# Kernel tuning notes

Hardware: AMD Instinct MI355X
Metric: run time of the kernel (lower is better)

Reference implementation:

```python
import jax, jax.numpy as jnp
import numpy as np

NUM_EXPERTS = 8


def setup_inputs() -> dict:
    key = jax.random.key(0)
    k1, k2 = jax.random.split(key)
    G, T, D, E = 4, 2048, 1024, NUM_EXPERTS
    token_inputs = jax.random.normal(k1, (G, T, D), dtype=jnp.float32)
    router_weight = jax.random.normal(k2, (E, D), dtype=jnp.float32) * 0.02
    router_bias = jnp.zeros((E,), dtype=jnp.float32)
    return {
        "token_inputs": token_inputs,
        "router_weight": router_weight,
        "router_bias": router_bias,
        "expert_capacity": 320,
    }


def _routing(probs, expert_capacities):
    """Experts-preferred assignment: experts pick tokens in order, each up to
    its capacity, from tokens not yet taken by earlier experts."""
    G, T, E = probs.shape
    max_cap = max(expert_capacities)
    dispatch = jnp.zeros((G, T, E, max_cap), dtype=jnp.int32)
    combine = jnp.zeros((G, T, E, max_cap), dtype=probs.dtype)
    available = jnp.ones((G, T), dtype=probs.dtype)  # 1 if token unassigned
    g_idx = jnp.arange(G)[:, None]
    for e, cap in enumerate(expert_capacities):  # static small loop over experts
        masked = probs[:, :, e] * available                 # [G, T]
        gate, idx = jax.lax.top_k(masked, cap)              # [G, cap]
        c_idx = jnp.arange(cap)[None, :]
        dispatch = dispatch.at[g_idx, idx, e, c_idx].set(1)
        combine = combine.at[g_idx, idx, e, c_idx].set(gate)
        available = available.at[g_idx, idx].set(0.0)       # chosen tokens now taken
    return dispatch, combine


def reference(token_inputs, router_weight, router_bias, expert_capacity):
    x = token_inputs.astype(jnp.float32)
    # router logits: [G, T, E]
    logits = jnp.einsum("gtd,ed->gte", x, router_weight) + router_bias
    probs = jax.nn.softmax(logits, axis=-1)
    capacities = [int(expert_capacity)] * NUM_EXPERTS
    dispatch_mask, combine_array = _routing(probs, capacities)
    # router z-loss: mean over groups*tokens of logsumexp(logits)^2
    log_z = jax.nn.logsumexp(logits, axis=-1)
    z_loss = jnp.sum(log_z ** 2) / (logits.shape[0] * logits.shape[1])
    auxiliary_loss = jnp.float32(0.0)
    router_causal_loss = jnp.float32(0.0)
    return dispatch_mask, combine_array, auxiliary_loss, z_loss, router_causal_loss
```

## Files before the change

kernel.cpp:

```cpp
#include <hip/hip_runtime.h>

#define NEXP 8
typedef unsigned long long u64;
typedef unsigned int u32;

__global__ __launch_bounds__(512) void probs_fill_kernel(
    const float* __restrict__ x,
    const float* __restrict__ w,
    const float* __restrict__ bias,
    float* __restrict__ probsT,
    double* __restrict__ zpart,
    int* __restrict__ flags,
    float* __restrict__ out,
    long long nout4,
    long long GT, int npb, int nfb)
{
    if (blockIdx.x == 0 && threadIdx.x < 8) flags[threadIdx.x] = 0;

    if ((int)blockIdx.x >= npb) {
        const int fb = (int)blockIdx.x - npb;
        const long long stride = (long long)nfb * 512;
        const float4 z = make_float4(0.f, 0.f, 0.f, 0.f);
        for (long long k = (long long)fb * 512 + threadIdx.x; k < nout4; k += stride) {
            reinterpret_cast<float4*>(out)[k] = z;
        }
        return;
    }

    __shared__ float wl[NEXP * 1024];
    __shared__ double zred[8];
    for (int i = threadIdx.x; i < NEXP * 1024 / 4; i += 512) {
        reinterpret_cast<float4*>(wl)[i] = reinterpret_cast<const float4*>(w)[i];
    }
    __syncthreads();

    const int wave = threadIdx.x >> 6;
    const int lane = threadIdx.x & 63;
    const long long t = (long long)blockIdx.x * 8 + wave;
    const float* xr = x + t * 1024;

    float acc[NEXP];
#pragma unroll
    for (int e = 0; e < NEXP; ++e) acc[e] = 0.f;

#pragma unroll
    for (int c = 0; c < 4; ++c) {
        const int d = c * 256 + lane * 4;
        const float4 xv = *reinterpret_cast<const float4*>(xr + d);
#pragma unroll
        for (int e = 0; e < NEXP; ++e) {
            const float4 wv = *reinterpret_cast<const float4*>(wl + e * 1024 + d);
            acc[e] = fmaf(xv.x, wv.x, acc[e]);
            acc[e] = fmaf(xv.y, wv.y, acc[e]);
            acc[e] = fmaf(xv.z, wv.z, acc[e]);
            acc[e] = fmaf(xv.w, wv.w, acc[e]);
        }
    }
#pragma unroll
    for (int e = 0; e < NEXP; ++e) {
#pragma unroll
        for (int off = 32; off; off >>= 1) acc[e] += __shfl_xor(acc[e], off, 64);
    }

    if (lane == 0) {
        double l[NEXP];
        double mx = -1e300;
#pragma unroll
        for (int e = 0; e < NEXP; ++e) {
            l[e] = (double)acc[e] + (double)bias[e];
            mx = fmax(mx, l[e]);
        }
        double ex[NEXP];
        double s = 0.0;
#pragma unroll
        for (int e = 0; e < NEXP; ++e) { ex[e] = exp(l[e] - mx); s += ex[e]; }
        const double inv = 1.0 / s;
#pragma unroll
        for (int e = 0; e < NEXP; ++e) probsT[(long long)e * GT + t] = (float)(ex[e] * inv);
        const double lse = mx + log(s);
        zred[wave] = lse * lse;
    }
    __syncthreads();
    if (threadIdx.x == 0) {
        double s = 0.0;
#pragma unroll
        for (int i = 0; i < 8; ++i) s += zred[i];
        zpart[blockIdx.x] = s;
    }
}

#define NRANK 256

union __align__(16) Smem2 {
    struct { u64 keys[2048]; int part[1024]; } b;
    struct { int avail[2048]; int cnt[32]; int cnt2[32]; } c;
};

__global__ __launch_bounds__(1024) void rank_assign_kernel(
    const float* __restrict__ probsT,
    u64* __restrict__ skey,
    int* __restrict__ flags,
    const double* __restrict__ zpart,
    int nzpart,
    float* __restrict__ out,
    int T, int G, int cap, long long GT)
{
    __shared__ Smem2 sm;
    const int b = blockIdx.x;
    const int tid = threadIdx.x;
    const int lane = tid & 63;
    const int wv = tid >> 6;

    if (b < NRANK) {
        const int pair = b >> 3;
        const int sub  = b & 7;
        const int e = pair / G;
        const int g = pair - e * G;
        const float* p = probsT + (long long)e * GT + (long long)g * T;
        for (int j = tid; j < 2048; j += 1024)
            sm.b.keys[j] = ((u64)__float_as_uint(p[j]) << 32) | (u32)(~(u32)j);
        __syncthreads();
        const int slot = tid & 255;
        const int q = tid >> 8;
        const u64 kt = sm.b.keys[sub * 256 + slot];
        const ulonglong2* k2 = reinterpret_cast<const ulonglong2*>(sm.b.keys) + q * 256;
        int r = 0;
#pragma unroll 8
        for (int j = 0; j < 256; ++j) {
            const ulonglong2 v = k2[j];
            r += (v.x > kt); r += (v.y > kt);
        }
        sm.b.part[tid] = r;
        __syncthreads();
        if (tid < 256) {
            const int rank = sm.b.part[tid] + sm.b.part[tid + 256] + sm.b.part[tid + 512] + sm.b.part[tid + 768];
            skey[(long long)pair * T + rank] = sm.b.keys[sub * 256 + tid];
        }
        __syncthreads();
        if (tid == 0) { __threadfence(); atomicAdd(&flags[g], 1); }
        return;
    }

    const int g = b - NRANK;
    if (tid == 0) {
        while (__hip_atomic_load(&flags[g], __ATOMIC_RELAXED, __HIP_MEMORY_SCOPE_AGENT) < 64)
            __builtin_amdgcn_s_sleep(2);
        __threadfence();
    }
    __syncthreads();

    u64 ka[NEXP], kb[NEXP];
#pragma unroll
    for (int e = 0; e < NEXP; ++e) {
        const long long base = (long long)(e * G + g) * T;
        ka[e] = skey[base + tid];
        kb[e] = skey[base + tid + 1024];
    }
    sm.c.avail[tid] = 1;
    sm.c.avail[tid + 1024] = 1;

    float* dispatch = out;
    float* combine  = out + GT * (long long)NEXP * cap;
    const long long gbase = (long long)g * T;
    const u64 lmask = (lane == 0) ? 0ull : ((~0ull) >> (64 - lane));

    for (int e = 0; e < NEXP; ++e) {
        __syncthreads();
        const u64 k0 = ka[e], k1 = kb[e];
        const u32 idx0 = ~(u32)k0, idx1 = ~(u32)k1;
        const float v0 = __uint_as_float((u32)(k0 >> 32));
        const float v1 = __uint_as_float((u32)(k1 >> 32));
        const int f0 = sm.c.avail[idx0];
        const int f1 = sm.c.avail[idx1];
        const u64 m0 = __ballot(f0);
        const u64 m1 = __ballot(f1);
        if (lane == 0) { sm.c.cnt[wv] = __popcll(m0); sm.c.cnt[16 + wv] = __popcll(m1); }
        __syncthreads();
        int vi = (lane < 32) ? sm.c.cnt[lane] : 0;
#pragma unroll
        for (int o = 1; o < 32; o <<= 1) { const int t2 = __shfl_up(vi, o, 64); if (lane >= o) vi += t2; }
        const int off0 = wv ? __shfl(vi, wv - 1, 64) : 0;
        const int off1 = __shfl(vi, 15 + wv, 64);
        const int S    = __shfl(vi, 31, 64);
        const int pre0 = off0 + __popcll(m0 & lmask);
        const int pre1 = off1 + __popcll(m1 & lmask);
        const bool s0 = f0 && (pre0 < cap);
        const bool s1 = f1 && (pre1 < cap);
        if (s0) { const long long o_ = ((gbase + idx0) * NEXP + e) * (long long)cap + pre0; dispatch[o_] = 1.0f; combine[o_] = v0; }
        if (s1) { const long long o_ = ((gbase + idx1) * NEXP + e) * (long long)cap + pre1; dispatch[o_] = 1.0f; combine[o_] = v1; }
        if (S < cap) {
            const int u0 = 1 - sm.c.avail[tid];
            const int u1 = 1 - sm.c.avail[tid + 1024];
            const u64 n0 = __ballot(u0);
            const u64 n1 = __ballot(u1);
            if (lane == 0) { sm.c.cnt2[wv] = __popcll(n0); sm.c.cnt2[16 + wv] = __popcll(n1); }
            __syncthreads();
            int vj = (lane < 32) ? sm.c.cnt2[lane] : 0;
#pragma unroll
            for (int o = 1; o < 32; o <<= 1) { const int t2 = __shfl_up(vj, o, 64); if (lane >= o) vj += t2; }
            const int qoff0 = wv ? __shfl(vj, wv - 1, 64) : 0;
            const int qoff1 = __shfl(vj, 15 + wv, 64);
            const int q0 = qoff0 + __popcll(n0 & lmask);
            const int q1 = qoff1 + __popcll(n1 & lmask);
            const int nfill = cap - S;
            if (u0 && q0 < nfill) { const long long o_ = ((gbase + tid) * NEXP + e) * (long long)cap + S + q0; dispatch[o_] = 1.0f; }
            if (u1 && q1 < nfill) { const long long o_ = ((gbase + tid + 1024) * NEXP + e) * (long long)cap + S + q1; dispatch[o_] = 1.0f; }
        }
        if (s0) sm.c.avail[idx0] = 0;
        if (s1) sm.c.avail[idx1] = 0;
    }

    if (g == 0 && tid < 64) {
        double s = 0.0;
        for (int i = tid; i < nzpart; i += 64) s += zpart[i];
#pragma unroll
        for (int o = 32; o; o >>= 1) s += __shfl_xor(s, o, 64);
        if (tid == 0) {
            float* sc = out + 2 * GT * (long long)NEXP * cap;
            sc[0] = 0.0f;
            sc[1] = (float)(s / (double)GT);
            sc[2] = 0.0f;
        }
    }
}

extern "C" void kernel_launch(void* const* d_in, const int* in_sizes, int n_in,
                              void* d_out, int out_size, void* d_ws, size_t ws_size,
                              hipStream_t stream) {
    (void)n_in; (void)ws_size;
    const float* x    = (const float*)d_in[0];
    const float* w    = (const float*)d_in[1];
    const float* bias = (const float*)d_in[2];

    const int E = in_sizes[2];
    const int D = in_sizes[1] / E;
    const long long GT = (long long)in_sizes[0] / D;
    const int T = 2048;
    const int G = (int)(GT / T);
    const int cap = (int)(((long long)out_size - 3) / (2 * GT * E));
    const int npb = (int)(GT / 8);
    const int nfb = 2048;

    int*    flags  = (int*)d_ws;
    double* zpart  = (double*)((char*)d_ws + 4096);
    float*  probsT = (float*)((char*)d_ws + 16384);
    u64*    skey   = (u64*)((char*)d_ws + 16384 + (size_t)E * GT * sizeof(float));

    const long long nout4 = ((long long)out_size - 3) >> 2;

    probs_fill_kernel<<<npb + nfb, 512, 0, stream>>>(
        x, w, bias, probsT, zpart, flags, (float*)d_out, nout4, GT, npb, nfb);

    rank_assign_kernel<<<NRANK + G, 1024, 0, stream>>>(
        probsT, skey, flags, zpart, npb, (float*)d_out, T, G, cap, GT);
}
```

Baseline: 71.15 us.

## Split output zero-fill across kernels and buffer assignments in LDS

The output zero-fill is split. The first kernel clears only the first 3/8 of the output, and 256 extra blocks in the second kernel clear the rest while the ranking and assignment work runs. The assign blocks no longer write dispatch and combine inside the expert loop. They record each (value, index) entry in an LDS buffer, wait on a flag counter until all fill blocks finish, then scatter the entries. This overlaps the memset traffic with the serial routing work, at the cost of extra LDS use, a cross-block spin-wait, and the split ratio chosen by hand.

```diff
diff --git a/kernel.cpp b/kernel.cpp
--- a/kernel.cpp
+++ b/kernel.cpp
@@ -1,6 +1,9 @@
 #include <hip/hip_runtime.h>
 
 #define NEXP 8
+#define NRANK 256
+#define NFB2 256
+#define MAXCAP 512
 typedef unsigned long long u64;
 typedef unsigned int u32;
 
@@ -12,7 +15,7 @@
     double* __restrict__ zpart,
     int* __restrict__ flags,
     float* __restrict__ out,
-    long long nout4,
+    long long split4,
     long long GT, int npb, int nfb)
 {
     if (blockIdx.x == 0 && threadIdx.x < 8) flags[threadIdx.x] = 0;
@@ -21,7 +24,7 @@
         const int fb = (int)blockIdx.x - npb;
         const long long stride = (long long)nfb * 512;
         const float4 z = make_float4(0.f, 0.f, 0.f, 0.f);
-        for (long long k = (long long)fb * 512 + threadIdx.x; k < nout4; k += stride) {
+        for (long long k = (long long)fb * 512 + threadIdx.x; k < split4; k += stride) {
             reinterpret_cast<float4*>(out)[k] = z;
         }
         return;
@@ -89,20 +92,20 @@
     }
 }
 
-#define NRANK 256
-
 union __align__(16) Smem2 {
     struct { u64 keys[2048]; int part[1024]; } b;
-    struct { int avail[2048]; int cnt[32]; int cnt2[32]; } c;
+    struct { int avail[2048]; int cnt[32]; int cnt2[32];
+             u64 cbuf[NEXP * MAXCAP]; } c;
 };
 
-__global__ __launch_bounds__(1024) void rank_assign_kernel(
+__global__ __launch_bounds__(1024) void rank_assign_fill_kernel(
     const float* __restrict__ probsT,
     u64* __restrict__ skey,
     int* __restrict__ flags,
     const double* __restrict__ zpart,
     int nzpart,
     float* __restrict__ out,
+    long long split4, long long nout4,
     int T, int G, int cap, long long GT)
 {
     __shared__ Smem2 sm;
@@ -110,6 +113,18 @@
     const int tid = threadIdx.x;
     const int lane = tid & 63;
     const int wv = tid >> 6;
+
+    if (b >= NRANK + G) {
+        const int fb = b - (NRANK + G);
+        const long long stride = (long long)NFB2 * 1024;
+        const float4 z = make_float4(0.f, 0.f, 0.f, 0.f);
+        for (long long k = split4 + (long long)fb * 1024 + tid; k < nout4; k += stride) {
+            reinterpret_cast<float4*>(out)[k] = z;
+        }
+        __syncthreads();
+        if (tid == 0) { __threadfence(); atomicAdd(&flags[4], 1); }
+        return;
+    }
 
     if (b < NRANK) {
         const int pair = b >> 3;
@@ -159,17 +174,12 @@
     sm.c.avail[tid] = 1;
     sm.c.avail[tid + 1024] = 1;
 
-    float* dispatch = out;
-    float* combine  = out + GT * (long long)NEXP * cap;
-    const long long gbase = (long long)g * T;
     const u64 lmask = (lane == 0) ? 0ull : ((~0ull) >> (64 - lane));
 
     for (int e = 0; e < NEXP; ++e) {
         __syncthreads();
         const u64 k0 = ka[e], k1 = kb[e];
         const u32 idx0 = ~(u32)k0, idx1 = ~(u32)k1;
-        const float v0 = __uint_as_float((u32)(k0 >> 32));
-        const float v1 = __uint_as_float((u32)(k1 >> 32));
         const int f0 = sm.c.avail[idx0];
         const int f1 = sm.c.avail[idx1];
         const u64 m0 = __ballot(f0);
@@ -186,8 +196,8 @@
         const int pre1 = off1 + __popcll(m1 & lmask);
         const bool s0 = f0 && (pre0 < cap);
         const bool s1 = f1 && (pre1 < cap);
-        if (s0) { const long long o_ = ((gbase + idx0) * NEXP + e) * (long long)cap + pre0; dispatch[o_] = 1.0f; combine[o_] = v0; }
-        if (s1) { const long long o_ = ((gbase + idx1) * NEXP + e) * (long long)cap + pre1; dispatch[o_] = 1.0f; combine[o_] = v1; }
+        if (s0) sm.c.cbuf[e * cap + pre0] = ((k0 >> 32) << 32) | (u64)idx0;
+        if (s1) sm.c.cbuf[e * cap + pre1] = ((k1 >> 32) << 32) | (u64)idx1;
         if (S < cap) {
             const int u0 = 1 - sm.c.avail[tid];
             const int u1 = 1 - sm.c.avail[tid + 1024];
@@ -203,12 +213,13 @@
             const int q0 = qoff0 + __popcll(n0 & lmask);
             const int q1 = qoff1 + __popcll(n1 & lmask);
             const int nfill = cap - S;
-            if (u0 && q0 < nfill) { const long long o_ = ((gbase + tid) * NEXP + e) * (long long)cap + S + q0; dispatch[o_] = 1.0f; }
-            if (u1 && q1 < nfill) { const long long o_ = ((gbase + tid + 1024) * NEXP + e) * (long long)cap + S + q1; dispatch[o_] = 1.0f; }
+            if (u0 && q0 < nfill) sm.c.cbuf[e * cap + S + q0] = (u64)(u32)tid;
+            if (u1 && q1 < nfill) sm.c.cbuf[e * cap + S + q1] = (u64)(u32)(tid + 1024);
         }
         if (s0) sm.c.avail[idx0] = 0;
         if (s1) sm.c.avail[idx1] = 0;
     }
+    __syncthreads();
 
     if (g == 0 && tid < 64) {
         double s = 0.0;
@@ -220,6 +231,28 @@
             sc[0] = 0.0f;
             sc[1] = (float)(s / (double)GT);
             sc[2] = 0.0f;
+        }
+    }
+
+    if (tid == 0) {
+        while (__hip_atomic_load(&flags[4], __ATOMIC_RELAXED, __HIP_MEMORY_SCOPE_AGENT) < NFB2)
+            __builtin_amdgcn_s_sleep(2);
+        __threadfence();
+    }
+    __syncthreads();
+
+    float* dispatch = out;
+    float* combine  = out + GT * (long long)NEXP * cap;
+    const long long gbase = (long long)g * T;
+#pragma unroll
+    for (int e = 0; e < NEXP; ++e) {
+        for (int c = tid; c < cap; c += 1024) {
+            const u64 en = sm.c.cbuf[e * cap + c];
+            const u32 idx = (u32)en;
+            const float val = __uint_as_float((u32)(en >> 32));
+            const long long o_ = ((gbase + idx) * NEXP + e) * (long long)cap + c;
+            dispatch[o_] = 1.0f;
+            combine[o_]  = val;
         }
     }
 }
@@ -247,10 +280,11 @@
     u64*    skey   = (u64*)((char*)d_ws + 16384 + (size_t)E * GT * sizeof(float));
 
     const long long nout4 = ((long long)out_size - 3) >> 2;
+    const long long split4 = (nout4 * 3) / 8;
 
     probs_fill_kernel<<<npb + nfb, 512, 0, stream>>>(
-        x, w, bias, probsT, zpart, flags, (float*)d_out, nout4, GT, npb, nfb);
-
-    rank_assign_kernel<<<NRANK + G, 1024, 0, stream>>>(
-        probsT, skey, flags, zpart, npb, (float*)d_out, T, G, cap, GT);
+        x, w, bias, probsT, zpart, flags, (float*)d_out, split4, GT, npb, nfb);
+
+    rank_assign_fill_kernel<<<NRANK + G + NFB2, 1024, 0, stream>>>(
+        probsT, skey, flags, zpart, npb, (float*)d_out, split4, nout4, T, G, cap, GT);
 }
```

Result: slower. 73.43 us (+3.2%).

## Run per-group greedy assignment on a single wavefront without block barriers

Applied to the files above, without the earlier changes.

The per-group assignment phase now runs on one 64-lane wave per group. Each expert's sorted keys are loaded into registers and processed in 32 chunks with running ballot prefix counts, replacing the 1024-thread version that needed several __syncthreads and cross-wave scans per expert. This removes barrier and shared-memory scan overhead from the serial expert loop, but each group's work is now serialized on a single wave and most of the block's threads return early. The z-loss block also zeroes any tail output elements not covered by the float4 fill.

```diff
diff --git a/kernel.cpp b/kernel.cpp
--- a/kernel.cpp
+++ b/kernel.cpp
@@ -1,6 +1,7 @@
 #include <hip/hip_runtime.h>
 
 #define NEXP 8
+#define NRANK 256
 typedef unsigned long long u64;
 typedef unsigned int u32;
 
@@ -89,11 +90,9 @@
     }
 }
 
-#define NRANK 256
-
 union __align__(16) Smem2 {
     struct { u64 keys[2048]; int part[1024]; } b;
-    struct { int avail[2048]; int cnt[32]; int cnt2[32]; } c;
+    struct { int avail[2048]; } c;
 };
 
 __global__ __launch_bounds__(1024) void rank_assign_kernel(
@@ -103,13 +102,12 @@
     const double* __restrict__ zpart,
     int nzpart,
     float* __restrict__ out,
+    long long nout4, int out_size,
     int T, int G, int cap, long long GT)
 {
     __shared__ Smem2 sm;
     const int b = blockIdx.x;
     const int tid = threadIdx.x;
-    const int lane = tid & 63;
-    const int wv = tid >> 6;
 
     if (b < NRANK) {
         const int pair = b >> 3;
@@ -123,11 +121,11 @@
         const int slot = tid & 255;
         const int q = tid >> 8;
         const u64 kt = sm.b.keys[sub * 256 + slot];
-        const ulonglong2* k2 = reinterpret_cast<const ulonglong2*>(sm.b.keys) + q * 256;
+        const ulonglong2* k2p = reinterpret_cast<const ulonglong2*>(sm.b.keys) + q * 256;
         int r = 0;
 #pragma unroll 8
         for (int j = 0; j < 256; ++j) {
-            const ulonglong2 v = k2[j];
+            const ulonglong2 v = k2p[j];
             r += (v.x > kt); r += (v.y > kt);
         }
         sm.b.part[tid] = r;
@@ -142,81 +140,79 @@
     }
 
     const int g = b - NRANK;
-    if (tid == 0) {
-        while (__hip_atomic_load(&flags[g], __ATOMIC_RELAXED, __HIP_MEMORY_SCOPE_AGENT) < 64)
-            __builtin_amdgcn_s_sleep(2);
-        __threadfence();
-    }
-    __syncthreads();
-
-    u64 ka[NEXP], kb[NEXP];
-#pragma unroll
-    for (int e = 0; e < NEXP; ++e) {
-        const long long base = (long long)(e * G + g) * T;
-        ka[e] = skey[base + tid];
-        kb[e] = skey[base + tid + 1024];
-    }
-    sm.c.avail[tid] = 1;
-    sm.c.avail[tid + 1024] = 1;
-
+    if (tid >= 64) return;
+    const int lane = tid;
+
+    while (__hip_atomic_load(&flags[g], __ATOMIC_RELAXED, __HIP_MEMORY_SCOPE_AGENT) < NRANK / 4)
+        __builtin_amdgcn_s_sleep(2);
+    __threadfence();
+
+    for (int j = lane; j < 2048; j += 64) sm.c.avail[j] = 1;
+
+    const u64 lmask = (lane == 0) ? 0ull : ((~0ull) >> (64 - lane));
+    const long long gbase = (long long)g * T;
     float* dispatch = out;
     float* combine  = out + GT * (long long)NEXP * cap;
-    const long long gbase = (long long)g * T;
-    const u64 lmask = (lane == 0) ? 0ull : ((~0ull) >> (64 - lane));
-
+
+    u64 kc[32];
+#pragma unroll 1
     for (int e = 0; e < NEXP; ++e) {
-        __syncthreads();
-        const u64 k0 = ka[e], k1 = kb[e];
-        const u32 idx0 = ~(u32)k0, idx1 = ~(u32)k1;
-        const float v0 = __uint_as_float((u32)(k0 >> 32));
-        const float v1 = __uint_as_float((u32)(k1 >> 32));
-        const int f0 = sm.c.avail[idx0];
-        const int f1 = sm.c.avail[idx1];
-        const u64 m0 = __ballot(f0);
-        const u64 m1 = __ballot(f1);
-        if (lane == 0) { sm.c.cnt[wv] = __popcll(m0); sm.c.cnt[16 + wv] = __popcll(m1); }
-        __syncthreads();
-        int vi = (lane < 32) ? sm.c.cnt[lane] : 0;
-#pragma unroll
-        for (int o = 1; o < 32; o <<= 1) { const int t2 = __shfl_up(vi, o, 64); if (lane >= o) vi += t2; }
-        const int off0 = wv ? __shfl(vi, wv - 1, 64) : 0;
-        const int off1 = __shfl(vi, 15 + wv, 64);
-        const int S    = __shfl(vi, 31, 64);
-        const int pre0 = off0 + __popcll(m0 & lmask);
-        const int pre1 = off1 + __popcll(m1 & lmask);
-        const bool s0 = f0 && (pre0 < cap);
-        const bool s1 = f1 && (pre1 < cap);
-        if (s0) { const long long o_ = ((gbase + idx0) * NEXP + e) * (long long)cap + pre0; dispatch[o_] = 1.0f; combine[o_] = v0; }
-        if (s1) { const long long o_ = ((gbase + idx1) * NEXP + e) * (long long)cap + pre1; dispatch[o_] = 1.0f; combine[o_] = v1; }
+        const long long kb = (long long)(e * G + g) * T;
+#pragma unroll
+        for (int c = 0; c < 32; ++c) kc[c] = skey[kb + c * 64 + lane];
+
+        u32 selmask = 0;
+        int scount = 0;
+#pragma unroll
+        for (int cc = 0; cc < 4; ++cc) {
+            int av[8];
+#pragma unroll
+            for (int j = 0; j < 8; ++j)
+                av[j] = sm.c.avail[(~(u32)kc[cc * 8 + j]) & 2047u];
+#pragma unroll
+            for (int j = 0; j < 8; ++j) {
+                const int c = cc * 8 + j;
+                const u64 m = __ballot(av[j] != 0);
+                const int pre = scount + __popcll(m & lmask);
+                if (av[j] && pre < cap) {
+                    const u32 idx = (~(u32)kc[c]) & 2047u;
+                    const long long o_ = ((gbase + idx) * NEXP + e) * (long long)cap + pre;
+                    dispatch[o_] = 1.0f;
+                    combine[o_]  = __uint_as_float((u32)(kc[c] >> 32));
+                    selmask |= (1u << c);
+                }
+                scount += __popcll(m);
+            }
+        }
+        const int S = scount;
         if (S < cap) {
-            const int u0 = 1 - sm.c.avail[tid];
-            const int u1 = 1 - sm.c.avail[tid + 1024];
-            const u64 n0 = __ballot(u0);
-            const u64 n1 = __ballot(u1);
-            if (lane == 0) { sm.c.cnt2[wv] = __popcll(n0); sm.c.cnt2[16 + wv] = __popcll(n1); }
-            __syncthreads();
-            int vj = (lane < 32) ? sm.c.cnt2[lane] : 0;
-#pragma unroll
-            for (int o = 1; o < 32; o <<= 1) { const int t2 = __shfl_up(vj, o, 64); if (lane >= o) vj += t2; }
-            const int qoff0 = wv ? __shfl(vj, wv - 1, 64) : 0;
-            const int qoff1 = __shfl(vj, 15 + wv, 64);
-            const int q0 = qoff0 + __popcll(n0 & lmask);
-            const int q1 = qoff1 + __popcll(n1 & lmask);
             const int nfill = cap - S;
-            if (u0 && q0 < nfill) { const long long o_ = ((gbase + tid) * NEXP + e) * (long long)cap + S + q0; dispatch[o_] = 1.0f; }
-            if (u1 && q1 < nfill) { const long long o_ = ((gbase + tid + 1024) * NEXP + e) * (long long)cap + S + q1; dispatch[o_] = 1.0f; }
-        }
-        if (s0) sm.c.avail[idx0] = 0;
-        if (s1) sm.c.avail[idx1] = 0;
-    }
-
-    if (g == 0 && tid < 64) {
+            int zc = 0;
+#pragma unroll
+            for (int c = 0; c < 32; ++c) {
+                const int un = (sm.c.avail[c * 64 + lane] == 0);
+                const u64 mn = __ballot(un);
+                const int qz = zc + __popcll(mn & lmask);
+                if (un && qz < nfill) {
+                    const long long o_ = ((gbase + c * 64 + lane) * NEXP + e) * (long long)cap + (S + qz);
+                    dispatch[o_] = 1.0f;
+                }
+                zc += __popcll(mn);
+            }
+        }
+#pragma unroll
+        for (int c = 0; c < 32; ++c)
+            if (selmask & (1u << c)) sm.c.avail[(~(u32)kc[c]) & 2047u] = 0;
+    }
+
+    if (g == 0) {
         double s = 0.0;
-        for (int i = tid; i < nzpart; i += 64) s += zpart[i];
+        for (int i = lane; i < nzpart; i += 64) s += zpart[i];
 #pragma unroll
         for (int o = 32; o; o >>= 1) s += __shfl_xor(s, o, 64);
-        if (tid == 0) {
+        if (lane == 0) {
             float* sc = out + 2 * GT * (long long)NEXP * cap;
+            for (long long j = nout4 * 4; j < (long long)out_size - 3; ++j) out[j] = 0.f;
             sc[0] = 0.0f;
             sc[1] = (float)(s / (double)GT);
             sc[2] = 0.0f;
@@ -252,5 +248,5 @@
         x, w, bias, probsT, zpart, flags, (float*)d_out, nout4, GT, npb, nfb);
 
     rank_assign_kernel<<<NRANK + G, 1024, 0, stream>>>(
-        probsT, skey, flags, zpart, npb, (float*)d_out, T, G, cap, GT);
+        probsT, skey, flags, zpart, npb, (float*)d_out, nout4, out_size, T, G, cap, GT);
 }
```

After: 92.60 us. 30.1% more time.
